# Optimization experiments

Measured on AMD Instinct MI355X. Metric: run time of the kernel, lower is better.

The kernel has to match this reference:

```python
import jax, jax.numpy as jnp
import numpy as np

N_NODES = 50000
N_EDGES = 800000
D = 64


def setup_inputs() -> dict:
    key = jax.random.key(0)
    k1, k2, k3 = jax.random.split(key, 3)
    x = jax.random.normal(k1, (N_NODES, D), dtype=jnp.float32)
    edge_index = jax.random.randint(k2, (2, N_EDGES), 0, N_NODES, dtype=jnp.int64)
    # GCNConv linear weight (PyG stores lin.weight [out, in]; we use [in, out])
    W = jax.random.normal(k3, (D, D), dtype=jnp.float32) * (1.0 / np.sqrt(D))
    b = jnp.zeros((D,), dtype=jnp.float32)
    return {"x": x, "edge_index": edge_index, "W": W, "b": b}


def reference(x, edge_index, W, b):
    # ResidualGCNLayer forward (eval mode: dropout = identity).
    # in_channels == out_channels -> skip_connection is Identity.
    N = x.shape[0]
    E = edge_index.shape[1]
    dtype = x.dtype

    # GCNConv with add_self_loops=True, improved=False (fill value 1.0)
    loop = jnp.arange(N, dtype=edge_index.dtype)
    row = jnp.concatenate([edge_index[0], loop])  # source nodes
    col = jnp.concatenate([edge_index[1], loop])  # destination nodes
    ew = jnp.ones((E + N,), dtype=dtype)          # edge weights (self-loop fill=1)

    # symmetric normalization: D^{-1/2} A_hat D^{-1/2}
    deg = jax.ops.segment_sum(ew, col, num_segments=N)
    dinv = jnp.where(deg > 0, jax.lax.rsqrt(deg), jnp.zeros_like(deg))
    norm = dinv[row] * ew * dinv[col]             # [E+N]

    h = x @ W                                     # [N, D] transform before propagate
    msg = norm[:, None] * h[row]                  # [E+N, D] gathered + scaled messages
    agg = jax.ops.segment_sum(msg, col, num_segments=N)  # scatter-add aggregate

    identity = x                                  # Identity skip (in == out)
    out = jax.nn.relu(agg + b) + identity         # ReLU + (eval) dropout + residual
    return out
```

## Files before the change

kernel.cpp:

```cpp
#include <hip/hip_runtime.h>
#include <hip/hip_bf16.h>

#define D 64
#define CAP 64
#define NXCD 8
#define EPT 4

typedef int v4i __attribute__((ext_vector_type(4)));

__device__ __forceinline__ float bf16lo(unsigned u) {
    u <<= 16; return __builtin_bit_cast(float, u);
}
__device__ __forceinline__ float bf16hi(unsigned u) {
    u &= 0xffff0000u; return __builtin_bit_cast(float, u);
}
__device__ __forceinline__ unsigned bf16_rne(float f) {
    unsigned u = __builtin_bit_cast(unsigned, f);
    u += 0x7fffu + ((u >> 16) & 1u);
    return u >> 16;
}
__device__ __forceinline__ unsigned pack_bf16(float a, float b) {
    return bf16_rne(a) | (bf16_rne(b) << 16);
}

__global__ void zero_cnt_kernel(int* __restrict__ cnt, int N) {
    int i = blockIdx.x * blockDim.x + threadIdx.x;
    if (i < N) cnt[i] = 0;
}

__global__ __launch_bounds__(256) void fill_csr_sliced_kernel(
        const int* __restrict__ row, const int* __restrict__ col,
        int* __restrict__ cnt, int* __restrict__ csr, int E, int N) {
    const int slice = blockIdx.x & (NXCD - 1);
    const int chunk = blockIdx.x >> 3;
    const int per = (N + NXCD - 1) / NXCD;
    const int lo = slice * per;
    const int hi = min(N, lo + per);

    const int e0 = (chunk * 256 + (int)threadIdx.x) * EPT;
    if (e0 + EPT <= E) {
        v4i c4 = __builtin_nontemporal_load((const v4i*)(col + e0));
        #pragma unroll
        for (int i = 0; i < EPT; ++i) {
            int c = c4[i];
            if (c >= lo && c < hi) {
                int r = __builtin_nontemporal_load(row + e0 + i);
                int pos = atomicAdd(&cnt[c], 1);
                if (pos < CAP) csr[c * CAP + pos] = r;
            }
        }
    } else {
        for (int i = 0; i < EPT; ++i) {
            int e = e0 + i;
            if (e < E) {
                int c = col[e];
                if (c >= lo && c < hi) {
                    int pos = atomicAdd(&cnt[c], 1);
                    if (pos < CAP) csr[c * CAP + pos] = row[e];
                }
            }
        }
    }
}

__global__ __launch_bounds__(256) void transform_kernel(
        const float* __restrict__ x, const float* __restrict__ W,
        const int* __restrict__ cnt, unsigned* __restrict__ h2b, int N) {
    __shared__ float Ws[D * D];
    __shared__ float xs[32][68];

    for (int i = threadIdx.x; i < D * D; i += 256) Ws[i] = W[i];

    const int l16 = threadIdx.x & 15;
    const int m   = threadIdx.x >> 4;
    const int base = blockIdx.x * 64;
    const float4* x4 = (const float4*)x;

    for (int pass = 0; pass < 2; ++pass) {
        int nb = base + pass * 32;
        __syncthreads();
        for (int i = threadIdx.x; i < 512; i += 256) {
            int r = i >> 4, seg = i & 15;
            int n = nb + r;
            float4 v = make_float4(0.f, 0.f, 0.f, 0.f);
            if (n < N) v = x4[n * 16 + seg];
            *(float4*)&xs[r][seg * 4] = v;
        }
        __syncthreads();

        float4 acc0 = make_float4(0.f, 0.f, 0.f, 0.f);
        float4 acc1 = make_float4(0.f, 0.f, 0.f, 0.f);
        #pragma unroll 4
        for (int k4 = 0; k4 < 16; ++k4) {
            float4 xv0 = *(const float4*)&xs[m][k4 * 4];
            float4 xv1 = *(const float4*)&xs[m + 16][k4 * 4];
            #pragma unroll
            for (int kk = 0; kk < 4; ++kk) {
                float4 w4 = *(const float4*)&Ws[(k4 * 4 + kk) * D + l16 * 4];
                float a0 = kk == 0 ? xv0.x : kk == 1 ? xv0.y : kk == 2 ? xv0.z : xv0.w;
                float a1 = kk == 0 ? xv1.x : kk == 1 ? xv1.y : kk == 2 ? xv1.z : xv1.w;
                acc0.x = fmaf(a0, w4.x, acc0.x); acc0.y = fmaf(a0, w4.y, acc0.y);
                acc0.z = fmaf(a0, w4.z, acc0.z); acc0.w = fmaf(a0, w4.w, acc0.w);
                acc1.x = fmaf(a1, w4.x, acc1.x); acc1.y = fmaf(a1, w4.y, acc1.y);
                acc1.z = fmaf(a1, w4.z, acc1.z); acc1.w = fmaf(a1, w4.w, acc1.w);
            }
        }

        int n0 = nb + m, n1 = nb + m + 16;
        if (n0 < N) {
            float dn = rsqrtf((float)(cnt[n0] + 1));
            uint2 p; p.x = pack_bf16(acc0.x * dn, acc0.y * dn);
            p.y = pack_bf16(acc0.z * dn, acc0.w * dn);
            ((uint2*)h2b)[n0 * 16 + l16] = p;
        }
        if (n1 < N) {
            float dn = rsqrtf((float)(cnt[n1] + 1));
            uint2 p; p.x = pack_bf16(acc1.x * dn, acc1.y * dn);
            p.y = pack_bf16(acc1.z * dn, acc1.w * dn);
            ((uint2*)h2b)[n1 * 16 + l16] = p;
        }
    }
}

__global__ __launch_bounds__(256) void agg_kernel(
        const float* __restrict__ x, const float* __restrict__ b,
        const unsigned* __restrict__ h2b, const int* __restrict__ cnt,
        const int* __restrict__ csr, float* __restrict__ out, int N) {
    int c = blockIdx.x * 4 + (threadIdx.x >> 6);
    if (c >= N) return;
    const int lane = threadIdx.x & 63;
    const int g = lane >> 4;
    const int l16 = lane & 15;

    const uint2* hb = (const uint2*)h2b;
    float4 acc = make_float4(0.f, 0.f, 0.f, 0.f);

    if (g == 0) {
        uint2 v = hb[c * 16 + l16];
        acc.x = bf16lo(v.x); acc.y = bf16hi(v.x);
        acc.z = bf16lo(v.y); acc.w = bf16hi(v.y);
    }

    int n = cnt[c]; n = n < CAP ? n : CAP;
    const int* cb = csr + c * CAP;
    for (int j = g; j < n; j += 4) {
        int r = cb[j];
        uint2 v = hb[r * 16 + l16];
        acc.x += bf16lo(v.x); acc.y += bf16hi(v.x);
        acc.z += bf16lo(v.y); acc.w += bf16hi(v.y);
    }

    acc.x += __shfl_xor(acc.x, 16); acc.y += __shfl_xor(acc.y, 16);
    acc.z += __shfl_xor(acc.z, 16); acc.w += __shfl_xor(acc.w, 16);
    acc.x += __shfl_xor(acc.x, 32); acc.y += __shfl_xor(acc.y, 32);
    acc.z += __shfl_xor(acc.z, 32); acc.w += __shfl_xor(acc.w, 32);

    if (lane < 16) {
        float dc = rsqrtf((float)(cnt[c] + 1));
        float4 bv = ((const float4*)b)[l16];
        float4 xv = ((const float4*)x)[c * 16 + l16];
        float4 o;
        o.x = fmaf(dc, acc.x, bv.x); o.x = o.x > 0.0f ? o.x : 0.0f; o.x += xv.x;
        o.y = fmaf(dc, acc.y, bv.y); o.y = o.y > 0.0f ? o.y : 0.0f; o.y += xv.y;
        o.z = fmaf(dc, acc.z, bv.z); o.z = o.z > 0.0f ? o.z : 0.0f; o.z += xv.z;
        o.w = fmaf(dc, acc.w, bv.w); o.w = o.w > 0.0f ? o.w : 0.0f; o.w += xv.w;
        ((float4*)out)[c * 16 + l16] = o;
    }
}

extern "C" void kernel_launch(void* const* d_in, const int* in_sizes, int n_in,
                              void* d_out, int out_size, void* d_ws, size_t ws_size,
                              hipStream_t stream) {
    const float* x   = (const float*)d_in[0];
    const int*   ei  = (const int*)d_in[1];
    const float* W   = (const float*)d_in[2];
    const float* b   = (const float*)d_in[3];
    float*       out = (float*)d_out;

    const int N = in_sizes[0] / D;
    const int E = in_sizes[1] / 2;
    const int* row = ei;
    const int* col = ei + E;

    int*      cnt = (int*)d_ws;
    unsigned* h2b = (unsigned*)(cnt + N);
    int*      csr = (int*)(h2b + (size_t)N * D / 2);

    zero_cnt_kernel<<<(N + 255) / 256, 256, 0, stream>>>(cnt, N);

    const int fill_chunks = (E + 256 * EPT - 1) / (256 * EPT);
    fill_csr_sliced_kernel<<<fill_chunks * NXCD, 256, 0, stream>>>(row, col, cnt, csr, E, N);

    transform_kernel<<<(N + 63) / 64, 256, 0, stream>>>(x, W, cnt, h2b, N);
    agg_kernel<<<(N + 3) / 4, 256, 0, stream>>>(x, b, h2b, cnt, csr, out, N);
}
```

Baseline: 165.4 us.

## Use XCC-aware work-stealing queues for sliced CSR fill

Replaces the static grid, where the block index set both destination slice and edge chunk, with a persistent 2048-block kernel. Each block reads its hardware XCC ID and first pulls chunks from the atomic queue for its own node slice, then steals from the other slices. The aim is to keep each slice's atomics and CSR writes in the L2 of one XCD while balancing load dynamically. In exchange it adds a global atomic and two block barriers per chunk, and it assumes the XCC ID register is available and that blocks are spread evenly across XCDs.

```diff
diff --git a/kernel.cpp b/kernel.cpp
--- a/kernel.cpp
+++ b/kernel.cpp
@@ -8,6 +8,12 @@
 
 typedef int v4i __attribute__((ext_vector_type(4)));
 
+__device__ __forceinline__ int get_xcc_id() {
+    unsigned v;
+    asm volatile("s_getreg_b32 %0, hwreg(HW_REG_XCC_ID)" : "=s"(v));
+    return (int)(v & (NXCD - 1));
+}
+
 __device__ __forceinline__ float bf16lo(unsigned u) {
     u <<= 16; return __builtin_bit_cast(float, u);
 }
@@ -23,40 +29,53 @@
     return bf16_rne(a) | (bf16_rne(b) << 16);
 }
 
-__global__ void zero_cnt_kernel(int* __restrict__ cnt, int N) {
+__global__ void zero_cnt_kernel(int* __restrict__ cnt, int* __restrict__ qcnt, int N) {
     int i = blockIdx.x * blockDim.x + threadIdx.x;
     if (i < N) cnt[i] = 0;
-}
-
-__global__ __launch_bounds__(256) void fill_csr_sliced_kernel(
+    if (i < NXCD) qcnt[i] = 0;
+}
+
+__global__ __launch_bounds__(256) void fill_csr_ws_kernel(
         const int* __restrict__ row, const int* __restrict__ col,
-        int* __restrict__ cnt, int* __restrict__ csr, int E, int N) {
-    const int slice = blockIdx.x & (NXCD - 1);
-    const int chunk = blockIdx.x >> 3;
+        int* __restrict__ cnt, int* __restrict__ csr,
+        int* __restrict__ qcnt, int E, int N, int nchunks) {
+    __shared__ int sh_chunk;
     const int per = (N + NXCD - 1) / NXCD;
-    const int lo = slice * per;
-    const int hi = min(N, lo + per);
-
-    const int e0 = (chunk * 256 + (int)threadIdx.x) * EPT;
-    if (e0 + EPT <= E) {
-        v4i c4 = __builtin_nontemporal_load((const v4i*)(col + e0));
-        #pragma unroll
-        for (int i = 0; i < EPT; ++i) {
-            int c = c4[i];
-            if (c >= lo && c < hi) {
-                int r = __builtin_nontemporal_load(row + e0 + i);
-                int pos = atomicAdd(&cnt[c], 1);
-                if (pos < CAP) csr[c * CAP + pos] = r;
-            }
-        }
-    } else {
-        for (int i = 0; i < EPT; ++i) {
-            int e = e0 + i;
-            if (e < E) {
-                int c = col[e];
-                if (c >= lo && c < hi) {
-                    int pos = atomicAdd(&cnt[c], 1);
-                    if (pos < CAP) csr[c * CAP + pos] = row[e];
+    const int xcc = get_xcc_id();
+
+    for (int pass = 0; pass < NXCD; ++pass) {
+        const int s = (xcc + pass) & (NXCD - 1);
+        const int lo = s * per;
+        const int hi = min(N, lo + per);
+        for (;;) {
+            if (threadIdx.x == 0) sh_chunk = atomicAdd(&qcnt[s], 1);
+            __syncthreads();
+            const int chunk = sh_chunk;
+            __syncthreads();
+            if (chunk >= nchunks) break;
+
+            const int e0 = (chunk * 256 + (int)threadIdx.x) * EPT;
+            if (e0 + EPT <= E) {
+                v4i c4 = __builtin_nontemporal_load((const v4i*)(col + e0));
+                #pragma unroll
+                for (int i = 0; i < EPT; ++i) {
+                    int c = c4[i];
+                    if (c >= lo && c < hi) {
+                        int r = __builtin_nontemporal_load(row + e0 + i);
+                        int pos = atomicAdd(&cnt[c], 1);
+                        if (pos < CAP) csr[c * CAP + pos] = r;
+                    }
+                }
+            } else {
+                for (int i = 0; i < EPT; ++i) {
+                    int e = e0 + i;
+                    if (e < E) {
+                        int c = col[e];
+                        if (c >= lo && c < hi) {
+                            int pos = atomicAdd(&cnt[c], 1);
+                            if (pos < CAP) csr[c * CAP + pos] = row[e];
+                        }
+                    }
                 }
             }
         }
@@ -185,11 +204,12 @@
     int*      cnt = (int*)d_ws;
     unsigned* h2b = (unsigned*)(cnt + N);
     int*      csr = (int*)(h2b + (size_t)N * D / 2);
-
-    zero_cnt_kernel<<<(N + 255) / 256, 256, 0, stream>>>(cnt, N);
-
-    const int fill_chunks = (E + 256 * EPT - 1) / (256 * EPT);
-    fill_csr_sliced_kernel<<<fill_chunks * NXCD, 256, 0, stream>>>(row, col, cnt, csr, E, N);
+    int*      qcnt = csr + (size_t)N * CAP;
+
+    zero_cnt_kernel<<<(N + 255) / 256, 256, 0, stream>>>(cnt, qcnt, N);
+
+    const int nchunks = (E + 256 * EPT - 1) / (256 * EPT);
+    fill_csr_ws_kernel<<<2048, 256, 0, stream>>>(row, col, cnt, csr, qcnt, E, N, nchunks);
 
     transform_kernel<<<(N + 63) / 64, 256, 0, stream>>>(x, W, cnt, h2b, N);
     agg_kernel<<<(N + 3) / 4, 256, 0, stream>>>(x, b, h2b, cnt, csr, out, N);
```

After: 395.4 us. +139.0%, slower.
